# Performance work log

Measured on AMD Instinct MI355X. Metric: run time of the kernel, lower is better.

Reference implementation:

```python
import math
import jax, jax.numpy as jnp
import numpy as np

B = 256          # graphs per batch
N0 = 512         # nodes per graph
DEG = 16         # avg degree
E = B * N0 * DEG # total edges
F_IN = 160
H = 64
RATIO = 0.11
NUM_CLASSES = 2


def setup_inputs() -> dict:
    key = jax.random.key(0)
    ks = jax.random.split(key, 20)
    x = jax.random.normal(ks[0], (B * N0, F_IN), jnp.float32)
    # within-graph random edges: src/dst local in [0, N0) plus graph offset
    eg = E // B
    off = (jnp.arange(B, dtype=jnp.int32) * N0)[:, None]
    src = (jax.random.randint(ks[1], (B, eg), 0, N0, jnp.int32) + off).reshape(-1)
    dst = (jax.random.randint(ks[2], (B, eg), 0, N0, jnp.int32) + off).reshape(-1)
    edge_index = jnp.stack([src, dst], 0)
    s = lambda fan: 1.0 / np.sqrt(fan)
    inp = {
        'x': x,
        'edge_index': edge_index,
        'conv1_Wr': jax.random.normal(ks[3], (F_IN, H), jnp.float32) * s(F_IN),
        'conv1_Wl': jax.random.normal(ks[4], (F_IN, H), jnp.float32) * s(F_IN),
        'conv1_b': jnp.zeros((H,), jnp.float32),
        'convs_Wr': jax.random.normal(ks[5], (5, H, H), jnp.float32) * s(H),
        'convs_Wl': jax.random.normal(ks[6], (5, H, H), jnp.float32) * s(H),
        'convs_b': jnp.zeros((5, H), jnp.float32),
        'pools_Wr': jax.random.normal(ks[7], (2, H, 1), jnp.float32) * s(H),
        'pools_Wl': jax.random.normal(ks[8], (2, H, 1), jnp.float32) * s(H),
        'pools_b': jnp.zeros((2, 1), jnp.float32),
        'lin1_W': jax.random.normal(ks[9], (6 * H, H), jnp.float32) * s(6 * H),
        'lin1_b': jnp.zeros((H,), jnp.float32),
        'lin2_W': jax.random.normal(ks[10], (H, NUM_CLASSES), jnp.float32) * s(H),
        'lin2_b': jnp.zeros((NUM_CLASSES,), jnp.float32),
    }
    return inp


def _gconv(x, src, dst, emask, Wr, Wl, b, n_nodes):
    # PyG GraphConv(aggr='mean'): lin_rel(mean_{j->i} x_j) + lin_root(x)
    msg = x[src] * emask[:, None]                              # [E, F]
    agg = jax.ops.segment_sum(msg, dst, num_segments=n_nodes)  # [N, F]
    deg = jax.ops.segment_sum(emask, dst, num_segments=n_nodes)
    agg = agg / jnp.maximum(deg, 1.0)[:, None]
    return agg @ Wr + b + x @ Wl


def _sag_pool(x, src, dst, emask, Wr, Wl, b, n_per, k):
    n_nodes = B * n_per
    score = _gconv(x, src, dst, emask, Wr, Wl, b, n_nodes)[:, 0]   # [N]
    _, idx = jax.lax.top_k(score.reshape(B, n_per), k)             # [B, k]
    perm = (idx + (jnp.arange(B, dtype=jnp.int32) * n_per)[:, None]).reshape(-1)
    new_x = x[perm] * jnp.tanh(score[perm])[:, None]
    newpos = jnp.full((n_nodes,), -1, jnp.int32).at[perm].set(
        jnp.arange(B * k, dtype=jnp.int32))
    ns, nd = newpos[src], newpos[dst]
    valid = (ns >= 0) & (nd >= 0)
    new_emask = emask * valid.astype(emask.dtype)
    return new_x, jnp.where(valid, ns, 0), jnp.where(valid, nd, 0), new_emask


def _gmp(x, n_per):  # global_mean_pool with equal-size graphs
    return x.reshape(B, n_per, -1).mean(axis=1)


def reference(x, edge_index, conv1_Wr, conv1_Wl, conv1_b, convs_Wr, convs_Wl,
              convs_b, pools_Wr, pools_Wl, pools_b, lin1_W, lin1_b,
              lin2_W, lin2_b):
    src, dst = edge_index[0], edge_index[1]
    emask = jnp.ones(src.shape, x.dtype)
    n = N0
    x = jax.nn.relu(_gconv(x, src, dst, emask, conv1_Wr, conv1_Wl, conv1_b, B * n))
    xs = [_gmp(x, n)]
    for i in range(5):
        x = jax.nn.relu(_gconv(x, src, dst, emask, convs_Wr[i], convs_Wl[i],
                               convs_b[i], B * n))
        xs.append(_gmp(x, n))
        if i % 2 == 0 and i < 4:
            j = i // 2
            k = math.ceil(RATIO * n)
            x, src, dst, emask = _sag_pool(x, src, dst, emask, pools_Wr[j],
                                           pools_Wl[j], pools_b[j], n, k)
            n = k
    h = jnp.concatenate(xs, axis=-1)          # JumpingKnowledge('cat') -> [B, 6H]
    h = jax.nn.relu(h @ lin1_W + lin1_b)
    h = h @ lin2_W + lin2_b                   # dropout is identity in eval mode
    return jax.nn.log_softmax(h, axis=-1)
```

## Files before the change

kernel.cpp:

```cpp
#include <hip/hip_runtime.h>
#include <math.h>

namespace {
constexpr int NB   = 256;
constexpr int EPG  = 8192;
constexpr int ETOT = NB * EPG;
constexpr int FH   = 64;
constexpr int NN0  = NB * 512;
}

__device__ float g_feat[3][(size_t)NN0 * FH];
__device__ float g_xs[NB * 6 * FH];
__device__ int   g_esrc[2][ETOT];
__device__ int   g_edst[2][ETOT];
__device__ int   g_ecnt[2][NB];
__device__ unsigned short g_csr[ETOT];
__device__ unsigned int   g_deg[NN0], g_start[NN0];

template<int K>
__global__ __launch_bounds__(256)
void mm_dual(const float* __restrict__ xext, int in_idx,
             const float* __restrict__ Wr, const float* __restrict__ Wl,
             const float* __restrict__ bias, int zr_idx, int xl_idx)
{
  constexpr int RPB = 64;
  constexpr int KC  = 32;
  __shared__ float xs[RPB][KC];
  __shared__ float wrT[KC/4][64][4];
  __shared__ float wlT[KC/4][64][4];
  const float* __restrict__ x = (in_idx < 0) ? xext : g_feat[in_idx];
  float* __restrict__ zr = g_feat[zr_idx];
  float* __restrict__ xl = g_feat[xl_idx];
  const int t = threadIdx.x;
  const int rowbase = blockIdx.x * RPB;
  const int f  = t & 31;
  const int rg = t >> 5;
  const int wv = t >> 6;
  const int wc = t & 63;
  const int wq = t >> 6;
  float ar0[8], ar1[8], al0[8], al1[8];
  #pragma unroll
  for (int r = 0; r < 8; ++r) { ar0[r]=0.f; ar1[r]=0.f; al0[r]=0.f; al1[r]=0.f; }

  for (int c = 0; c < K / KC; ++c) {
    __syncthreads();
    #pragma unroll
    for (int i = 0; i < 2; ++i) {
      const int idx = t + i * 256;
      const int r = idx >> 3, q = idx & 7;
      const float* gp = &x[(size_t)(rowbase + r) * K + c * KC + q * 4];
      float* lp = &xs[0][0] + (size_t)(i * 256 + wv * 64) * 4;
      __builtin_amdgcn_global_load_lds(
          (const __attribute__((address_space(1))) unsigned int*)gp,
          (__attribute__((address_space(3))) unsigned int*)lp, 16, 0, 0);
    }
    #pragma unroll
    for (int h = 0; h < 2; ++h) {
      const int kq = wq * 2 + h;
      #pragma unroll
      for (int i = 0; i < 4; ++i) {
        const int krow = c * KC + kq * 4 + i;
        wrT[kq][wc][i] = Wr[(size_t)krow * 64 + wc];
        wlT[kq][wc][i] = Wl[(size_t)krow * 64 + wc];
      }
    }
    __syncthreads();
    #pragma unroll 1
    for (int k4 = 0; k4 < KC / 4; ++k4) {
      const float4 wr0 = *reinterpret_cast<const float4*>(&wrT[k4][f][0]);
      const float4 wr1 = *reinterpret_cast<const float4*>(&wrT[k4][f+32][0]);
      const float4 wl0 = *reinterpret_cast<const float4*>(&wlT[k4][f][0]);
      const float4 wl1 = *reinterpret_cast<const float4*>(&wlT[k4][f+32][0]);
      #pragma unroll
      for (int r = 0; r < 8; ++r) {
        const float4 xv = *reinterpret_cast<const float4*>(&xs[rg*8 + r][k4*4]);
        float a0 = ar0[r], a1 = ar1[r], b0 = al0[r], b1 = al1[r];
        a0 = fmaf(xv.x, wr0.x, a0); a0 = fmaf(xv.y, wr0.y, a0);
        a0 = fmaf(xv.z, wr0.z, a0); a0 = fmaf(xv.w, wr0.w, a0);
        a1 = fmaf(xv.x, wr1.x, a1); a1 = fmaf(xv.y, wr1.y, a1);
        a1 = fmaf(xv.z, wr1.z, a1); a1 = fmaf(xv.w, wr1.w, a1);
        b0 = fmaf(xv.x, wl0.x, b0); b0 = fmaf(xv.y, wl0.y, b0);
        b0 = fmaf(xv.z, wl0.z, b0); b0 = fmaf(xv.w, wl0.w, b0);
        b1 = fmaf(xv.x, wl1.x, b1); b1 = fmaf(xv.y, wl1.y, b1);
        b1 = fmaf(xv.z, wl1.z, b1); b1 = fmaf(xv.w, wl1.w, b1);
        ar0[r] = a0; ar1[r] = a1; al0[r] = b0; al1[r] = b1;
      }
    }
  }
  const float bv0 = bias[f], bv1 = bias[f + 32];
  #pragma unroll
  for (int r = 0; r < 8; ++r) {
    const size_t row = (size_t)(rowbase + rg * 8 + r);
    zr[row * 64 + f]      = ar0[r];
    zr[row * 64 + f + 32] = ar1[r];
    xl[row * 64 + f]      = al0[r] + bv0;
    xl[row * 64 + f + 32] = al1[r] + bv1;
  }
}

__global__ __launch_bounds__(1024)
void agg_full_build(int zr_idx, int xl_idx,
                    const int* __restrict__ esrc, const int* __restrict__ edst,
                    int out_idx, int xs_off)
{
  __shared__ float zlds[512 * 64];
  __shared__ unsigned short csr[EPG];
  __shared__ unsigned int hist[512], bufA[512], bufB[512];
  __shared__ float red[16][64];
  const float* __restrict__ zr  = g_feat[zr_idx];
  const float* __restrict__ xlb = g_feat[xl_idx];
  float* __restrict__ xout = g_feat[out_idx];
  const int g = blockIdx.x, t = threadIdx.x;
  const int gbase = g * 512, ebase = g * EPG;
  if (t < 512) hist[t] = 0;
  __syncthreads();
  {
    const float4* zsrc = reinterpret_cast<const float4*>(zr + (size_t)gbase * 64);
    float4* zdst = reinterpret_cast<float4*>(zlds);
    #pragma unroll
    for (int i = 0; i < 8; ++i) zdst[t + i * 1024] = zsrc[t + i * 1024];
  }
  for (int e = t; e < EPG; e += 1024)
    atomicAdd(&hist[edst[ebase + e] - gbase], 1u);
  __syncthreads();
  if (t < 512) bufA[t] = hist[t];
  __syncthreads();
  unsigned int *pa = bufA, *pb = bufB;
  for (int off = 1; off < 512; off <<= 1) {
    if (t < 512) {
      unsigned int v = pa[t];
      if (t >= off) v += pa[t - off];
      pb[t] = v;
    }
    __syncthreads();
    unsigned int* tmp = pa; pa = pb; pb = tmp;
  }
  unsigned int excl = 0;
  if (t < 512) excl = pa[t] - hist[t];
  __syncthreads();
  if (t < 512) { bufA[t] = excl; bufB[t] = excl; }
  __syncthreads();
  for (int e = t; e < EPG; e += 1024) {
    const int sl = esrc[ebase + e] - gbase;
    const int dl = edst[ebase + e] - gbase;
    const unsigned int pos = atomicAdd(&bufB[dl], 1u);
    csr[pos] = (unsigned short)sl;
  }
  __syncthreads();
  if (t < 512) { g_deg[gbase + t] = hist[t]; g_start[gbase + t] = bufA[t]; }
  {
    unsigned int* gcsr32 = reinterpret_cast<unsigned int*>(&g_csr[ebase]);
    const unsigned int* lcsr32 = reinterpret_cast<const unsigned int*>(csr);
    for (int i = t; i < EPG/2; i += 1024) gcsr32[i] = lcsr32[i];
  }
  const int lane = t & 63, w = t >> 6;
  float psum = 0.f;
  for (int nd = w; nd < 512; nd += 16) {
    const unsigned int s = bufA[nd], d = hist[nd];
    float a0 = 0.f, a1 = 0.f, a2 = 0.f, a3 = 0.f;
    unsigned int j = 0;
    for (; j + 4 <= d; j += 4) {
      const int i0 = csr[s+j], i1 = csr[s+j+1], i2 = csr[s+j+2], i3 = csr[s+j+3];
      a0 += zlds[i0*64 + lane]; a1 += zlds[i1*64 + lane];
      a2 += zlds[i2*64 + lane]; a3 += zlds[i3*64 + lane];
    }
    for (; j < d; ++j) a0 += zlds[csr[s+j]*64 + lane];
    const float acc = (a0 + a1) + (a2 + a3);
    float v = acc / (float)(d > 0 ? d : 1) + xlb[(size_t)(gbase + nd)*64 + lane];
    v = fmaxf(v, 0.f);
    xout[(size_t)(gbase + nd)*64 + lane] = v;
    psum += v;
  }
  red[w][lane] = psum;
  __syncthreads();
  if (t < 64) {
    float s = 0.f;
    #pragma unroll
    for (int ww = 0; ww < 16; ++ww) s += red[ww][t];
    g_xs[g*384 + xs_off + t] = s * (1.f/512.f);
  }
}

__global__ __launch_bounds__(1024)
void conv_agg_pool(int x_idx, const float* __restrict__ Wr,
                   const float* __restrict__ Wl, const float* __restrict__ bias,
                   const int* __restrict__ esrc, const int* __restrict__ edst,
                   const float* __restrict__ pwr, const float* __restrict__ pwl,
                   const float* __restrict__ pb,
                   int xnew_idx, int xs_off)
{
  __shared__ float zlds[512 * 64];
  __shared__ unsigned short csrbuf[EPG];
  __shared__ __align__(16) unsigned long long u2[512];
  __shared__ float wpf[2048];
  __shared__ int scnt;
  unsigned int* hist  = reinterpret_cast<unsigned int*>(u2);
  unsigned int* start = hist + 512;
  const float* __restrict__ X1 = g_feat[x_idx];
  float* __restrict__ xnew = g_feat[xnew_idx];
  const int g = blockIdx.x, t = threadIdx.x;
  const int gbase = g * 512, ebase = g * EPG;
  const int lane = t & 63, w = t >> 6;
  const int ndbase = w * 32;
  {
    const float4* src = reinterpret_cast<const float4*>(X1 + (size_t)gbase * 64);
    float4* dst = reinterpret_cast<float4*>(zlds);
    #pragma unroll
    for (int i = 0; i < 8; ++i) dst[t + i * 1024] = src[t + i * 1024];
  }
  if (t < 512) { hist[t] = g_deg[gbase + t]; start[t] = g_start[gbase + t]; }
  {
    const uint4* c4 = reinterpret_cast<const uint4*>(&g_csr[ebase]);
    uint4* l4 = reinterpret_cast<uint4*>(csrbuf);
    l4[t] = c4[t];
  }
  if (t == 0) scnt = 0;
  float zacc[32], xla[32];
  #pragma unroll
  for (int i = 0; i < 32; ++i) { zacc[i] = 0.f; xla[i] = 0.f; }
  float* w_r = wpf;
  float* w_l = wpf + 1024;
  #pragma unroll 1
  for (int c = 0; c < 4; ++c) {
    __syncthreads();
    w_r[t] = Wr[c * 1024 + t];
    w_l[t] = Wl[c * 1024 + t];
    __syncthreads();
    #pragma unroll 1
    for (int k4 = 0; k4 < 4; ++k4) {
      const int kb = k4 * 4;
      const float wr0 = w_r[(kb+0)*64 + lane], wr1 = w_r[(kb+1)*64 + lane],
                  wr2 = w_r[(kb+2)*64 + lane], wr3 = w_r[(kb+3)*64 + lane];
      const float wl0 = w_l[(kb+0)*64 + lane], wl1 = w_l[(kb+1)*64 + lane],
                  wl2 = w_l[(kb+2)*64 + lane], wl3 = w_l[(kb+3)*64 + lane];
      #pragma unroll
      for (int i = 0; i < 32; ++i) {
        const float4 xv = *reinterpret_cast<const float4*>(
            &zlds[(ndbase + i) * 64 + c * 16 + kb]);
        float za = zacc[i], xa = xla[i];
        za = fmaf(xv.x, wr0, za); za = fmaf(xv.y, wr1, za);
        za = fmaf(xv.z, wr2, za); za = fmaf(xv.w, wr3, za);
        xa = fmaf(xv.x, wl0, xa); xa = fmaf(xv.y, wl1, xa);
        xa = fmaf(xv.z, wl2, xa); xa = fmaf(xv.w, wl3, xa);
        zacc[i] = za; xla[i] = xa;
      }
    }
  }
  __syncthreads();
  #pragma unroll
  for (int i = 0; i < 32; ++i)
    zlds[(ndbase + i) * 64 + lane] = zacc[i];
  __syncthreads();
  const float bv = bias[lane];
  float psum = 0.f;
  #pragma unroll 1
  for (int i = 0; i < 32; ++i) {
    const int nd = ndbase + i;
    const unsigned int s = start[nd], d = hist[nd];
    float a0 = 0.f, a1 = 0.f, a2 = 0.f, a3 = 0.f;
    unsigned int j = 0;
    for (; j + 4 <= d; j += 4) {
      const int i0 = csrbuf[s+j], i1 = csrbuf[s+j+1],
                i2 = csrbuf[s+j+2], i3 = csrbuf[s+j+3];
      a0 += zlds[i0*64 + lane]; a1 += zlds[i1*64 + lane];
      a2 += zlds[i2*64 + lane]; a3 += zlds[i3*64 + lane];
    }
    for (; j < d; ++j) a0 += zlds[csrbuf[s+j]*64 + lane];
    float v = ((a0 + a1) + (a2 + a3)) / (float)(d > 0 ? d : 1) + xla[i] + bv;
    v = fmaxf(v, 0.f);
    zacc[i] = v;
    psum += v;
  }
  __syncthreads();
  #pragma unroll
  for (int i = 0; i < 32; ++i)
    zlds[(ndbase + i) * 64 + lane] = zacc[i];
  wpf[w * 64 + lane] = psum;
  __syncthreads();
  if (t < 64) {
    float s = 0.f;
    #pragma unroll
    for (int ww = 0; ww < 16; ++ww) s += wpf[ww*64 + t];
    g_xs[g*384 + xs_off + t] = s * (1.f/512.f);
  }
  __syncthreads();
  float* zs     = wpf;
  float* swl    = wpf + 512;
  float* sscore = wpf + 1024;
  const float pwrv = pwr[lane], pwlv = pwl[lane];
  for (int nd = w; nd < 512; nd += 16) {
    const float v = zlds[nd*64 + lane];
    float a = v * pwrv, b = v * pwlv;
    #pragma unroll
    for (int off = 32; off > 0; off >>= 1) {
      a += __shfl_xor(a, off);
      b += __shfl_xor(b, off);
    }
    if (lane == 0) { zs[nd] = a; swl[nd] = b; }
  }
  __syncthreads();
  if (t < 512) {
    const unsigned int s = start[t], d = hist[t];
    float a = 0.f;
    for (unsigned int j = 0; j < d; ++j) a += zs[csrbuf[s + j]];
    sscore[t] = a / fmaxf((float)d, 1.f) + pb[0] + swl[t];
  }
  __syncthreads();
  unsigned long long* keys = u2;
  if (t < 512) {
    unsigned int u = __float_as_uint(sscore[t]);
    u = (u & 0x80000000u) ? ~u : (u | 0x80000000u);
    keys[t] = ((unsigned long long)u << 32) | (unsigned int)(~(unsigned int)t);
  }
  __syncthreads();
  for (int kk = 2; kk <= 512; kk <<= 1) {
    for (int j = kk >> 1; j > 0; j >>= 1) {
      if (t < 512) {
        const int ixj = t ^ j;
        if (ixj > t) {
          const unsigned long long a = keys[t], bk = keys[ixj];
          const bool up = ((t & kk) == 0);
          if (up ? (a < bk) : (a > bk)) { keys[t] = bk; keys[ixj] = a; }
        }
      }
      __syncthreads();
    }
  }
  short* np = reinterpret_cast<short*>(csrbuf);
  if (t < 512) np[t] = -1;
  __syncthreads();
  if (t < 57)
    np[(int)(~(unsigned int)(keys[t] & 0xffffffffull))] = (short)t;
  __syncthreads();
  for (int r = w; r < 57; r += 16) {
    const int old = (int)(~(unsigned int)(keys[r] & 0xffffffffull));
    const float sc = tanhf(sscore[old]);
    xnew[(size_t)(g*57 + r)*64 + lane] = zlds[old*64 + lane] * sc;
  }
  for (int e = t; e < EPG; e += 1024) {
    const int sl = esrc[ebase + e] - gbase;
    const int dl = edst[ebase + e] - gbase;
    const int ns = np[sl], nd2 = np[dl];
    if (ns >= 0 && nd2 >= 0) {
      const int slot = atomicAdd(&scnt, 1);
      g_esrc[0][ebase + slot] = g*57 + ns;
      g_edst[0][ebase + slot] = g*57 + nd2;
    }
  }
  __syncthreads();
  if (t == 0) g_ecnt[0][g] = scnt;
}

__device__ __forceinline__ void conv_small(
    float* X, float* Z, float* ACC, float* w_s, const float* deg,
    const float* Wr, const float* Wl, const float* bias,
    int n, const int* esrc, const int* edst, int m, int gb, int ebase,
    int xs_off, int g, int t, int lane, int w)
{
  for (int i = t; i < n*64; i += 512) { Z[i] = 0.f; ACC[i] = 0.f; }
  __syncthreads();
  for (int kc = 0; kc < 4; ++kc) {
    for (int i = t; i < 1024; i += 512) w_s[i] = Wr[kc*1024 + i];
    __syncthreads();
    for (int r = w; r < n; r += 8) {
      float zacc = 0.f;
      #pragma unroll
      for (int k = 0; k < 16; ++k)
        zacc = fmaf(X[r*64 + kc*16 + k], w_s[k*64 + lane], zacc);
      Z[r*64 + lane] += zacc;
    }
    __syncthreads();
  }
  for (int e = w; e < m; e += 8) {
    const int sl = esrc[ebase + e] - gb;
    const int dl = edst[ebase + e] - gb;
    atomicAdd(&ACC[dl*64 + lane], Z[sl*64 + lane]);
  }
  __syncthreads();
  for (int i = t; i < n*64; i += 512) {
    const int r = i >> 6, f = i & 63;
    Z[i] = ACC[i] / fmaxf(deg[r], 1.f) + bias[f];
  }
  __syncthreads();
  for (int kc = 0; kc < 4; ++kc) {
    for (int i = t; i < 1024; i += 512) w_s[i] = Wl[kc*1024 + i];
    __syncthreads();
    for (int r = w; r < n; r += 8) {
      float zacc = 0.f;
      #pragma unroll
      for (int k = 0; k < 16; ++k)
        zacc = fmaf(X[r*64 + kc*16 + k], w_s[k*64 + lane], zacc);
      Z[r*64 + lane] += zacc;
    }
    __syncthreads();
  }
  for (int i = t; i < n*64; i += 512) X[i] = fmaxf(Z[i], 0.f);
  __syncthreads();
  if (t < 64) {
    float s = 0.f;
    for (int r = 0; r < n; ++r) s += X[r*64 + t];
    g_xs[g*384 + xs_off + t] = s / (float)n;
  }
  __syncthreads();
}

__global__ __launch_bounds__(512)
void tail(const float* __restrict__ cWr, const float* __restrict__ cWl,
          const float* __restrict__ cb,
          const float* __restrict__ pWr, const float* __restrict__ pWl,
          const float* __restrict__ pb)
{
  __shared__ float X[57*64], Z[57*64], ACC[57*64];
  __shared__ float w_s[16*64];
  __shared__ float deg[64];
  __shared__ float zs[64], swl[64], sagg[64], sscore[64];
  __shared__ unsigned long long keys[64];
  __shared__ short newpos[64];
  __shared__ int scnt;
  const int g = blockIdx.x, t = threadIdx.x;
  const int lane = t & 63, w = t >> 6;
  const int ebase = g * EPG;

  for (int i = t; i < 57*64; i += 512) X[i] = g_feat[0][(size_t)(g*57)*64 + i];
  const int m0 = g_ecnt[0][g];
  if (t < 64) deg[t] = 0.f;
  __syncthreads();
  for (int e = t; e < m0; e += 512)
    atomicAdd(&deg[g_edst[0][ebase + e] - g*57], 1.f);
  __syncthreads();

  conv_small(X, Z, ACC, w_s, deg, cWr + 4096,  cWl + 4096,  cb + 64,
             57, g_esrc[0], g_edst[0], m0, g*57, ebase, 128, g, t, lane, w);
  conv_small(X, Z, ACC, w_s, deg, cWr + 8192,  cWl + 8192,  cb + 128,
             57, g_esrc[0], g_edst[0], m0, g*57, ebase, 192, g, t, lane, w);

  {
    const float pwrv = pWr[64 + lane], pwlv = pWl[64 + lane];
    for (int r = w; r < 57; r += 8) {
      float a = X[r*64 + lane] * pwrv, b = X[r*64 + lane] * pwlv;
      #pragma unroll
      for (int off = 32; off > 0; off >>= 1) {
        a += __shfl_xor(a, off);
        b += __shfl_xor(b, off);
      }
      if (lane == 0) { zs[r] = a; swl[r] = b; }
    }
    if (t < 64) sagg[t] = 0.f;
    if (t == 0) scnt = 0;
    __syncthreads();
    for (int e = t; e < m0; e += 512)
      atomicAdd(&sagg[g_edst[0][ebase + e] - g*57],
                zs[g_esrc[0][ebase + e] - g*57]);
    __syncthreads();
    if (t < 57) sscore[t] = sagg[t] / fmaxf(deg[t], 1.f) + pb[1] + swl[t];
    __syncthreads();
    if (t < 64) {
      unsigned long long key = 0ull;
      if (t < 57) {
        unsigned int u = __float_as_uint(sscore[t]);
        u = (u & 0x80000000u) ? ~u : (u | 0x80000000u);
        key = ((unsigned long long)u << 32) | (unsigned int)(~(unsigned int)t);
      }
      keys[t] = key;
    }
    __syncthreads();
    for (int kk = 2; kk <= 64; kk <<= 1) {
      for (int j = kk >> 1; j > 0; j >>= 1) {
        if (t < 64) {
          const int ixj = t ^ j;
          if (ixj > t) {
            const unsigned long long a = keys[t], bk = keys[ixj];
            const bool up = ((t & kk) == 0);
            if (up ? (a < bk) : (a > bk)) { keys[t] = bk; keys[ixj] = a; }
          }
        }
        __syncthreads();
      }
    }
    if (t < 64) newpos[t] = -1;
    __syncthreads();
    if (t < 7)
      newpos[(int)(~(unsigned int)(keys[t] & 0xffffffffull))] = (short)t;
    __syncthreads();
    for (int r = w; r < 7; r += 8) {
      const int old = (int)(~(unsigned int)(keys[r] & 0xffffffffull));
      const float sc = tanhf(sscore[old]);
      Z[r*64 + lane] = X[old*64 + lane] * sc;
    }
    for (int e = t; e < m0; e += 512) {
      const int sl = g_esrc[0][ebase + e] - g*57;
      const int dl = g_edst[0][ebase + e] - g*57;
      const int ns = newpos[sl], nd2 = newpos[dl];
      if (ns >= 0 && nd2 >= 0) {
        const int slot = atomicAdd(&scnt, 1);
        g_esrc[1][ebase + slot] = g*7 + ns;
        g_edst[1][ebase + slot] = g*7 + nd2;
      }
    }
    __syncthreads();
    for (int i = t; i < 7*64; i += 512) X[i] = Z[i];
    if (t < 64) deg[t] = 0.f;
    __syncthreads();
  }
  const int m1 = scnt;
  for (int e = t; e < m1; e += 512)
    atomicAdd(&deg[g_edst[1][ebase + e] - g*7], 1.f);
  __syncthreads();

  conv_small(X, Z, ACC, w_s, deg, cWr + 12288, cWl + 12288, cb + 192,
             7, g_esrc[1], g_edst[1], m1, g*7, ebase, 256, g, t, lane, w);
  conv_small(X, Z, ACC, w_s, deg, cWr + 16384, cWl + 16384, cb + 256,
             7, g_esrc[1], g_edst[1], m1, g*7, ebase, 320, g, t, lane, w);
}

__global__ __launch_bounds__(64)
void head(const float* __restrict__ W1, const float* __restrict__ b1,
          const float* __restrict__ W2, const float* __restrict__ b2,
          float* __restrict__ out)
{
  __shared__ float h[384], o1[64], lg[2];
  const int g = blockIdx.x, t = threadIdx.x;
  for (int i = t; i < 384; i += 64) h[i] = g_xs[g*384 + i];
  __syncthreads();
  float acc = b1[t];
  for (int j = 0; j < 384; ++j) acc = fmaf(h[j], W1[j*64 + t], acc);
  o1[t] = fmaxf(acc, 0.f);
  __syncthreads();
  if (t < 2) {
    float a2 = b2[t];
    for (int f2 = 0; f2 < 64; ++f2) a2 = fmaf(o1[f2], W2[f2*2 + t], a2);
    lg[t] = a2;
  }
  __syncthreads();
  if (t < 2) {
    const float mx = fmaxf(lg[0], lg[1]);
    const float lse = mx + logf(expf(lg[0]-mx) + expf(lg[1]-mx));
    out[g*2 + t] = lg[t] - lse;
  }
}

extern "C" void kernel_launch(void* const* d_in, const int* in_sizes, int n_in,
                              void* d_out, int out_size, void* d_ws, size_t ws_size,
                              hipStream_t stream)
{
  (void)in_sizes; (void)n_in; (void)d_ws; (void)ws_size; (void)out_size;
  const float* x    = (const float*)d_in[0];
  const int*   ei   = (const int*)d_in[1];
  const float* c1Wr = (const float*)d_in[2];
  const float* c1Wl = (const float*)d_in[3];
  const float* c1b  = (const float*)d_in[4];
  const float* cWr  = (const float*)d_in[5];
  const float* cWl  = (const float*)d_in[6];
  const float* cb   = (const float*)d_in[7];
  const float* pWr  = (const float*)d_in[8];
  const float* pWl  = (const float*)d_in[9];
  const float* pb   = (const float*)d_in[10];
  const float* l1W  = (const float*)d_in[11];
  const float* l1b  = (const float*)d_in[12];
  const float* l2W  = (const float*)d_in[13];
  const float* l2b  = (const float*)d_in[14];
  float* out = (float*)d_out;
  const int* esrc = ei;
  const int* edst = ei + ETOT;

  mm_dual<160><<<NN0/64, 256, 0, stream>>>(x, -1, c1Wr, c1Wl, c1b, 0, 1);
  agg_full_build<<<NB, 1024, 0, stream>>>(0, 1, esrc, edst, 1, 0);
  conv_agg_pool<<<NB, 1024, 0, stream>>>(1, cWr, cWl, cb, esrc, edst,
                                         pWr, pWl, pb, 0, 64);
  tail<<<NB, 512, 0, stream>>>(cWr, cWl, cb, pWr, pWl, pb);
  head<<<NB, 64, 0, stream>>>(l1W, l1b, l2W, l2b, out);
}
```

Measured before the change: 341.2 us.

## Fuse first conv matmul, CSR build and second conv into one per-graph kernel

Replaces the separate mm_dual, agg_full_build and conv_agg_pool launches with a single per-graph kernel. That kernel builds the CSR in LDS, computes the first-layer matmul from x streamed into LDS, aggregates, then runs the second conv and pool. This removes global round trips for intermediate features (zr, xl, x1), CSR and degree arrays, plus two launches. The cost is that the 160-wide matmul now runs on only 256 blocks of 1024 threads at one block per CU, which lowers parallelism compared with the 2048-block mm_dual.

```diff
diff --git a/kernel.cpp b/kernel.cpp
--- a/kernel.cpp
+++ b/kernel.cpp
@@ -9,185 +9,21 @@
 constexpr int NN0  = NB * 512;
 }
 
-__device__ float g_feat[3][(size_t)NN0 * FH];
+__device__ float g_feat[1][(size_t)NN0 * FH];
 __device__ float g_xs[NB * 6 * FH];
 __device__ int   g_esrc[2][ETOT];
 __device__ int   g_edst[2][ETOT];
 __device__ int   g_ecnt[2][NB];
-__device__ unsigned short g_csr[ETOT];
-__device__ unsigned int   g_deg[NN0], g_start[NN0];
-
-template<int K>
-__global__ __launch_bounds__(256)
-void mm_dual(const float* __restrict__ xext, int in_idx,
-             const float* __restrict__ Wr, const float* __restrict__ Wl,
-             const float* __restrict__ bias, int zr_idx, int xl_idx)
-{
-  constexpr int RPB = 64;
-  constexpr int KC  = 32;
-  __shared__ float xs[RPB][KC];
-  __shared__ float wrT[KC/4][64][4];
-  __shared__ float wlT[KC/4][64][4];
-  const float* __restrict__ x = (in_idx < 0) ? xext : g_feat[in_idx];
-  float* __restrict__ zr = g_feat[zr_idx];
-  float* __restrict__ xl = g_feat[xl_idx];
-  const int t = threadIdx.x;
-  const int rowbase = blockIdx.x * RPB;
-  const int f  = t & 31;
-  const int rg = t >> 5;
-  const int wv = t >> 6;
-  const int wc = t & 63;
-  const int wq = t >> 6;
-  float ar0[8], ar1[8], al0[8], al1[8];
-  #pragma unroll
-  for (int r = 0; r < 8; ++r) { ar0[r]=0.f; ar1[r]=0.f; al0[r]=0.f; al1[r]=0.f; }
-
-  for (int c = 0; c < K / KC; ++c) {
-    __syncthreads();
-    #pragma unroll
-    for (int i = 0; i < 2; ++i) {
-      const int idx = t + i * 256;
-      const int r = idx >> 3, q = idx & 7;
-      const float* gp = &x[(size_t)(rowbase + r) * K + c * KC + q * 4];
-      float* lp = &xs[0][0] + (size_t)(i * 256 + wv * 64) * 4;
-      __builtin_amdgcn_global_load_lds(
-          (const __attribute__((address_space(1))) unsigned int*)gp,
-          (__attribute__((address_space(3))) unsigned int*)lp, 16, 0, 0);
-    }
-    #pragma unroll
-    for (int h = 0; h < 2; ++h) {
-      const int kq = wq * 2 + h;
-      #pragma unroll
-      for (int i = 0; i < 4; ++i) {
-        const int krow = c * KC + kq * 4 + i;
-        wrT[kq][wc][i] = Wr[(size_t)krow * 64 + wc];
-        wlT[kq][wc][i] = Wl[(size_t)krow * 64 + wc];
-      }
-    }
-    __syncthreads();
-    #pragma unroll 1
-    for (int k4 = 0; k4 < KC / 4; ++k4) {
-      const float4 wr0 = *reinterpret_cast<const float4*>(&wrT[k4][f][0]);
-      const float4 wr1 = *reinterpret_cast<const float4*>(&wrT[k4][f+32][0]);
-      const float4 wl0 = *reinterpret_cast<const float4*>(&wlT[k4][f][0]);
-      const float4 wl1 = *reinterpret_cast<const float4*>(&wlT[k4][f+32][0]);
-      #pragma unroll
-      for (int r = 0; r < 8; ++r) {
-        const float4 xv = *reinterpret_cast<const float4*>(&xs[rg*8 + r][k4*4]);
-        float a0 = ar0[r], a1 = ar1[r], b0 = al0[r], b1 = al1[r];
-        a0 = fmaf(xv.x, wr0.x, a0); a0 = fmaf(xv.y, wr0.y, a0);
-        a0 = fmaf(xv.z, wr0.z, a0); a0 = fmaf(xv.w, wr0.w, a0);
-        a1 = fmaf(xv.x, wr1.x, a1); a1 = fmaf(xv.y, wr1.y, a1);
-        a1 = fmaf(xv.z, wr1.z, a1); a1 = fmaf(xv.w, wr1.w, a1);
-        b0 = fmaf(xv.x, wl0.x, b0); b0 = fmaf(xv.y, wl0.y, b0);
-        b0 = fmaf(xv.z, wl0.z, b0); b0 = fmaf(xv.w, wl0.w, b0);
-        b1 = fmaf(xv.x, wl1.x, b1); b1 = fmaf(xv.y, wl1.y, b1);
-        b1 = fmaf(xv.z, wl1.z, b1); b1 = fmaf(xv.w, wl1.w, b1);
-        ar0[r] = a0; ar1[r] = a1; al0[r] = b0; al1[r] = b1;
-      }
-    }
-  }
-  const float bv0 = bias[f], bv1 = bias[f + 32];
-  #pragma unroll
-  for (int r = 0; r < 8; ++r) {
-    const size_t row = (size_t)(rowbase + rg * 8 + r);
-    zr[row * 64 + f]      = ar0[r];
-    zr[row * 64 + f + 32] = ar1[r];
-    xl[row * 64 + f]      = al0[r] + bv0;
-    xl[row * 64 + f + 32] = al1[r] + bv1;
-  }
-}
 
 __global__ __launch_bounds__(1024)
-void agg_full_build(int zr_idx, int xl_idx,
-                    const int* __restrict__ esrc, const int* __restrict__ edst,
-                    int out_idx, int xs_off)
-{
-  __shared__ float zlds[512 * 64];
-  __shared__ unsigned short csr[EPG];
-  __shared__ unsigned int hist[512], bufA[512], bufB[512];
-  __shared__ float red[16][64];
-  const float* __restrict__ zr  = g_feat[zr_idx];
-  const float* __restrict__ xlb = g_feat[xl_idx];
-  float* __restrict__ xout = g_feat[out_idx];
-  const int g = blockIdx.x, t = threadIdx.x;
-  const int gbase = g * 512, ebase = g * EPG;
-  if (t < 512) hist[t] = 0;
-  __syncthreads();
-  {
-    const float4* zsrc = reinterpret_cast<const float4*>(zr + (size_t)gbase * 64);
-    float4* zdst = reinterpret_cast<float4*>(zlds);
-    #pragma unroll
-    for (int i = 0; i < 8; ++i) zdst[t + i * 1024] = zsrc[t + i * 1024];
-  }
-  for (int e = t; e < EPG; e += 1024)
-    atomicAdd(&hist[edst[ebase + e] - gbase], 1u);
-  __syncthreads();
-  if (t < 512) bufA[t] = hist[t];
-  __syncthreads();
-  unsigned int *pa = bufA, *pb = bufB;
-  for (int off = 1; off < 512; off <<= 1) {
-    if (t < 512) {
-      unsigned int v = pa[t];
-      if (t >= off) v += pa[t - off];
-      pb[t] = v;
-    }
-    __syncthreads();
-    unsigned int* tmp = pa; pa = pb; pb = tmp;
-  }
-  unsigned int excl = 0;
-  if (t < 512) excl = pa[t] - hist[t];
-  __syncthreads();
-  if (t < 512) { bufA[t] = excl; bufB[t] = excl; }
-  __syncthreads();
-  for (int e = t; e < EPG; e += 1024) {
-    const int sl = esrc[ebase + e] - gbase;
-    const int dl = edst[ebase + e] - gbase;
-    const unsigned int pos = atomicAdd(&bufB[dl], 1u);
-    csr[pos] = (unsigned short)sl;
-  }
-  __syncthreads();
-  if (t < 512) { g_deg[gbase + t] = hist[t]; g_start[gbase + t] = bufA[t]; }
-  {
-    unsigned int* gcsr32 = reinterpret_cast<unsigned int*>(&g_csr[ebase]);
-    const unsigned int* lcsr32 = reinterpret_cast<const unsigned int*>(csr);
-    for (int i = t; i < EPG/2; i += 1024) gcsr32[i] = lcsr32[i];
-  }
-  const int lane = t & 63, w = t >> 6;
-  float psum = 0.f;
-  for (int nd = w; nd < 512; nd += 16) {
-    const unsigned int s = bufA[nd], d = hist[nd];
-    float a0 = 0.f, a1 = 0.f, a2 = 0.f, a3 = 0.f;
-    unsigned int j = 0;
-    for (; j + 4 <= d; j += 4) {
-      const int i0 = csr[s+j], i1 = csr[s+j+1], i2 = csr[s+j+2], i3 = csr[s+j+3];
-      a0 += zlds[i0*64 + lane]; a1 += zlds[i1*64 + lane];
-      a2 += zlds[i2*64 + lane]; a3 += zlds[i3*64 + lane];
-    }
-    for (; j < d; ++j) a0 += zlds[csr[s+j]*64 + lane];
-    const float acc = (a0 + a1) + (a2 + a3);
-    float v = acc / (float)(d > 0 ? d : 1) + xlb[(size_t)(gbase + nd)*64 + lane];
-    v = fmaxf(v, 0.f);
-    xout[(size_t)(gbase + nd)*64 + lane] = v;
-    psum += v;
-  }
-  red[w][lane] = psum;
-  __syncthreads();
-  if (t < 64) {
-    float s = 0.f;
-    #pragma unroll
-    for (int ww = 0; ww < 16; ++ww) s += red[ww][t];
-    g_xs[g*384 + xs_off + t] = s * (1.f/512.f);
-  }
-}
-
-__global__ __launch_bounds__(1024)
-void conv_agg_pool(int x_idx, const float* __restrict__ Wr,
-                   const float* __restrict__ Wl, const float* __restrict__ bias,
-                   const int* __restrict__ esrc, const int* __restrict__ edst,
-                   const float* __restrict__ pwr, const float* __restrict__ pwl,
-                   const float* __restrict__ pb,
-                   int xnew_idx, int xs_off)
+void front(const float* __restrict__ x,
+           const int* __restrict__ esrc, const int* __restrict__ edst,
+           const float* __restrict__ c1Wr, const float* __restrict__ c1Wl,
+           const float* __restrict__ c1b,
+           const float* __restrict__ cWr, const float* __restrict__ cWl,
+           const float* __restrict__ cb,
+           const float* __restrict__ pwr, const float* __restrict__ pwl,
+           const float* __restrict__ pb)
 {
   __shared__ float zlds[512 * 64];
   __shared__ unsigned short csrbuf[EPG];
@@ -196,47 +32,79 @@
   __shared__ int scnt;
   unsigned int* hist  = reinterpret_cast<unsigned int*>(u2);
   unsigned int* start = hist + 512;
-  const float* __restrict__ X1 = g_feat[x_idx];
-  float* __restrict__ xnew = g_feat[xnew_idx];
+  float* __restrict__ xnew = g_feat[0];
   const int g = blockIdx.x, t = threadIdx.x;
   const int gbase = g * 512, ebase = g * EPG;
   const int lane = t & 63, w = t >> 6;
   const int ndbase = w * 32;
+
+  if (t < 512) hist[t] = 0;
+  if (t == 0) scnt = 0;
+  __syncthreads();
+  for (int e = t; e < EPG; e += 1024)
+    atomicAdd(&hist[edst[ebase + e] - gbase], 1u);
+  __syncthreads();
   {
-    const float4* src = reinterpret_cast<const float4*>(X1 + (size_t)gbase * 64);
-    float4* dst = reinterpret_cast<float4*>(zlds);
-    #pragma unroll
-    for (int i = 0; i < 8; ++i) dst[t + i * 1024] = src[t + i * 1024];
-  }
-  if (t < 512) { hist[t] = g_deg[gbase + t]; start[t] = g_start[gbase + t]; }
-  {
-    const uint4* c4 = reinterpret_cast<const uint4*>(&g_csr[ebase]);
-    uint4* l4 = reinterpret_cast<uint4*>(csrbuf);
-    l4[t] = c4[t];
-  }
-  if (t == 0) scnt = 0;
+    unsigned int* sA = reinterpret_cast<unsigned int*>(wpf);
+    unsigned int* sB = sA + 512;
+    if (t < 512) sA[t] = hist[t];
+    __syncthreads();
+    unsigned int *pa = sA, *pb = sB;
+    for (int off = 1; off < 512; off <<= 1) {
+      if (t < 512) {
+        unsigned int v = pa[t];
+        if (t >= off) v += pa[t - off];
+        pb[t] = v;
+      }
+      __syncthreads();
+      unsigned int* tmp = pa; pa = pb; pb = tmp;
+    }
+    if (t < 512) start[t] = pa[t] - hist[t];
+    __syncthreads();
+    unsigned int* cur = pb;
+    if (t < 512) cur[t] = start[t];
+    __syncthreads();
+    for (int e = t; e < EPG; e += 1024) {
+      const int sl = esrc[ebase + e] - gbase;
+      const int dl = edst[ebase + e] - gbase;
+      const unsigned int pos = atomicAdd(&cur[dl], 1u);
+      csrbuf[pos] = (unsigned short)sl;
+    }
+  }
   float zacc[32], xla[32];
   #pragma unroll
   for (int i = 0; i < 32; ++i) { zacc[i] = 0.f; xla[i] = 0.f; }
-  float* w_r = wpf;
-  float* w_l = wpf + 1024;
+  constexpr int WRO = 16384;
+  constexpr int WLO = 18432;
   #pragma unroll 1
-  for (int c = 0; c < 4; ++c) {
-    __syncthreads();
-    w_r[t] = Wr[c * 1024 + t];
-    w_l[t] = Wl[c * 1024 + t];
+  for (int c = 0; c < 5; ++c) {
+    __syncthreads();
+    #pragma unroll
+    for (int i = 0; i < 4; ++i) {
+      const int slot = t + i * 1024;
+      const int r = slot >> 3, q = slot & 7;
+      const float* gp = &x[(size_t)(gbase + r) * 160 + c * 32 + q * 4];
+      float* lp = zlds + (size_t)(i * 1024 + w * 64) * 4;
+      __builtin_amdgcn_global_load_lds(
+          (const __attribute__((address_space(1))) unsigned int*)gp,
+          (__attribute__((address_space(3))) unsigned int*)lp, 16, 0, 0);
+    }
+    zlds[WRO + t]        = c1Wr[c * 2048 + t];
+    zlds[WRO + 1024 + t] = c1Wr[c * 2048 + 1024 + t];
+    zlds[WLO + t]        = c1Wl[c * 2048 + t];
+    zlds[WLO + 1024 + t] = c1Wl[c * 2048 + 1024 + t];
     __syncthreads();
     #pragma unroll 1
-    for (int k4 = 0; k4 < 4; ++k4) {
+    for (int k4 = 0; k4 < 8; ++k4) {
       const int kb = k4 * 4;
-      const float wr0 = w_r[(kb+0)*64 + lane], wr1 = w_r[(kb+1)*64 + lane],
-                  wr2 = w_r[(kb+2)*64 + lane], wr3 = w_r[(kb+3)*64 + lane];
-      const float wl0 = w_l[(kb+0)*64 + lane], wl1 = w_l[(kb+1)*64 + lane],
-                  wl2 = w_l[(kb+2)*64 + lane], wl3 = w_l[(kb+3)*64 + lane];
+      const float wr0 = zlds[WRO + (kb+0)*64 + lane], wr1 = zlds[WRO + (kb+1)*64 + lane],
+                  wr2 = zlds[WRO + (kb+2)*64 + lane], wr3 = zlds[WRO + (kb+3)*64 + lane];
+      const float wl0 = zlds[WLO + (kb+0)*64 + lane], wl1 = zlds[WLO + (kb+1)*64 + lane],
+                  wl2 = zlds[WLO + (kb+2)*64 + lane], wl3 = zlds[WLO + (kb+3)*64 + lane];
       #pragma unroll
       for (int i = 0; i < 32; ++i) {
         const float4 xv = *reinterpret_cast<const float4*>(
-            &zlds[(ndbase + i) * 64 + c * 16 + kb]);
+            &zlds[(ndbase + i) * 32 + kb]);
         float za = zacc[i], xa = xla[i];
         za = fmaf(xv.x, wr0, za); za = fmaf(xv.y, wr1, za);
         za = fmaf(xv.z, wr2, za); za = fmaf(xv.w, wr3, za);
@@ -251,39 +119,112 @@
   for (int i = 0; i < 32; ++i)
     zlds[(ndbase + i) * 64 + lane] = zacc[i];
   __syncthreads();
-  const float bv = bias[lane];
-  float psum = 0.f;
-  #pragma unroll 1
-  for (int i = 0; i < 32; ++i) {
-    const int nd = ndbase + i;
-    const unsigned int s = start[nd], d = hist[nd];
-    float a0 = 0.f, a1 = 0.f, a2 = 0.f, a3 = 0.f;
-    unsigned int j = 0;
-    for (; j + 4 <= d; j += 4) {
-      const int i0 = csrbuf[s+j], i1 = csrbuf[s+j+1],
-                i2 = csrbuf[s+j+2], i3 = csrbuf[s+j+3];
-      a0 += zlds[i0*64 + lane]; a1 += zlds[i1*64 + lane];
-      a2 += zlds[i2*64 + lane]; a3 += zlds[i3*64 + lane];
-    }
-    for (; j < d; ++j) a0 += zlds[csrbuf[s+j]*64 + lane];
-    float v = ((a0 + a1) + (a2 + a3)) / (float)(d > 0 ? d : 1) + xla[i] + bv;
-    v = fmaxf(v, 0.f);
-    zacc[i] = v;
-    psum += v;
+  {
+    const float bv = c1b[lane];
+    float psum = 0.f;
+    #pragma unroll 1
+    for (int i = 0; i < 32; ++i) {
+      const int nd = ndbase + i;
+      const unsigned int s = start[nd], d = hist[nd];
+      float a0 = 0.f, a1 = 0.f, a2 = 0.f, a3 = 0.f;
+      unsigned int j = 0;
+      for (; j + 4 <= d; j += 4) {
+        const int i0 = csrbuf[s+j], i1 = csrbuf[s+j+1],
+                  i2 = csrbuf[s+j+2], i3 = csrbuf[s+j+3];
+        a0 += zlds[i0*64 + lane]; a1 += zlds[i1*64 + lane];
+        a2 += zlds[i2*64 + lane]; a3 += zlds[i3*64 + lane];
+      }
+      for (; j < d; ++j) a0 += zlds[csrbuf[s+j]*64 + lane];
+      float v = ((a0 + a1) + (a2 + a3)) / (float)(d > 0 ? d : 1) + xla[i] + bv;
+      v = fmaxf(v, 0.f);
+      zacc[i] = v;
+      psum += v;
+    }
+    __syncthreads();
+    #pragma unroll
+    for (int i = 0; i < 32; ++i)
+      zlds[(ndbase + i) * 64 + lane] = zacc[i];
+    wpf[w * 64 + lane] = psum;
+    __syncthreads();
+    if (t < 64) {
+      float s = 0.f;
+      #pragma unroll
+      for (int ww = 0; ww < 16; ++ww) s += wpf[ww*64 + t];
+      g_xs[g*384 + 0 + t] = s * (1.f/512.f);
+    }
+  }
+  #pragma unroll
+  for (int i = 0; i < 32; ++i) { zacc[i] = 0.f; xla[i] = 0.f; }
+  {
+    float* w_r = wpf;
+    float* w_l = wpf + 1024;
+    #pragma unroll 1
+    for (int c = 0; c < 4; ++c) {
+      __syncthreads();
+      w_r[t] = cWr[c * 1024 + t];
+      w_l[t] = cWl[c * 1024 + t];
+      __syncthreads();
+      #pragma unroll 1
+      for (int k4 = 0; k4 < 4; ++k4) {
+        const int kb = k4 * 4;
+        const float wr0 = w_r[(kb+0)*64 + lane], wr1 = w_r[(kb+1)*64 + lane],
+                    wr2 = w_r[(kb+2)*64 + lane], wr3 = w_r[(kb+3)*64 + lane];
+        const float wl0 = w_l[(kb+0)*64 + lane], wl1 = w_l[(kb+1)*64 + lane],
+                    wl2 = w_l[(kb+2)*64 + lane], wl3 = w_l[(kb+3)*64 + lane];
+        #pragma unroll
+        for (int i = 0; i < 32; ++i) {
+          const float4 xv = *reinterpret_cast<const float4*>(
+              &zlds[(ndbase + i) * 64 + c * 16 + kb]);
+          float za = zacc[i], xa = xla[i];
+          za = fmaf(xv.x, wr0, za); za = fmaf(xv.y, wr1, za);
+          za = fmaf(xv.z, wr2, za); za = fmaf(xv.w, wr3, za);
+          xa = fmaf(xv.x, wl0, xa); xa = fmaf(xv.y, wl1, xa);
+          xa = fmaf(xv.z, wl2, xa); xa = fmaf(xv.w, wl3, xa);
+          zacc[i] = za; xla[i] = xa;
+        }
+      }
+    }
   }
   __syncthreads();
   #pragma unroll
   for (int i = 0; i < 32; ++i)
     zlds[(ndbase + i) * 64 + lane] = zacc[i];
-  wpf[w * 64 + lane] = psum;
-  __syncthreads();
-  if (t < 64) {
-    float s = 0.f;
+  __syncthreads();
+  {
+    const float bv = cb[lane];
+    float psum = 0.f;
+    #pragma unroll 1
+    for (int i = 0; i < 32; ++i) {
+      const int nd = ndbase + i;
+      const unsigned int s = start[nd], d = hist[nd];
+      float a0 = 0.f, a1 = 0.f, a2 = 0.f, a3 = 0.f;
+      unsigned int j = 0;
+      for (; j + 4 <= d; j += 4) {
+        const int i0 = csrbuf[s+j], i1 = csrbuf[s+j+1],
+                  i2 = csrbuf[s+j+2], i3 = csrbuf[s+j+3];
+        a0 += zlds[i0*64 + lane]; a1 += zlds[i1*64 + lane];
+        a2 += zlds[i2*64 + lane]; a3 += zlds[i3*64 + lane];
+      }
+      for (; j < d; ++j) a0 += zlds[csrbuf[s+j]*64 + lane];
+      float v = ((a0 + a1) + (a2 + a3)) / (float)(d > 0 ? d : 1) + xla[i] + bv;
+      v = fmaxf(v, 0.f);
+      zacc[i] = v;
+      psum += v;
+    }
+    __syncthreads();
     #pragma unroll
-    for (int ww = 0; ww < 16; ++ww) s += wpf[ww*64 + t];
-    g_xs[g*384 + xs_off + t] = s * (1.f/512.f);
-  }
-  __syncthreads();
+    for (int i = 0; i < 32; ++i)
+      zlds[(ndbase + i) * 64 + lane] = zacc[i];
+    wpf[w * 64 + lane] = psum;
+    __syncthreads();
+    if (t < 64) {
+      float s = 0.f;
+      #pragma unroll
+      for (int ww = 0; ww < 16; ++ww) s += wpf[ww*64 + t];
+      g_xs[g*384 + 64 + t] = s * (1.f/512.f);
+    }
+    __syncthreads();
+  }
   float* zs     = wpf;
   float* swl    = wpf + 512;
   float* sscore = wpf + 1024;
@@ -563,10 +504,8 @@
   const int* esrc = ei;
   const int* edst = ei + ETOT;
 
-  mm_dual<160><<<NN0/64, 256, 0, stream>>>(x, -1, c1Wr, c1Wl, c1b, 0, 1);
-  agg_full_build<<<NB, 1024, 0, stream>>>(0, 1, esrc, edst, 1, 0);
-  conv_agg_pool<<<NB, 1024, 0, stream>>>(1, cWr, cWl, cb, esrc, edst,
-                                         pWr, pWl, pb, 0, 64);
+  front<<<NB, 1024, 0, stream>>>(x, esrc, edst, c1Wr, c1Wl, c1b,
+                                 cWr, cWl, cb, pWr, pWl, pb);
   tail<<<NB, 512, 0, stream>>>(cWr, cWl, cb, pWr, pWl, pb);
   head<<<NB, 64, 0, stream>>>(l1W, l1b, l2W, l2b, out);
 }
```

Result: no change. 336.1 us (-1.5%).
